# Kernel tuning notes

Measured on AMD Instinct MI355X. Metric: run time of the kernel, lower is better.

Reference implementation:

```python
import jax, jax.numpy as jnp
import numpy as np

ANCHORS = np.array([[10., 13.], [16., 30.], [33., 23.]], dtype=np.float32)
NUM_CLASSES = 80
IMG_W, IMG_H = 416, 416
IGNORE_THR = 0.5
OBJ_SCALE, NOOBJ_SCALE = 1.0, 0.5
EPS = 1e-12


def setup_inputs() -> dict:
    key = jax.random.key(0)
    k1, k2, k3, k4, k5 = jax.random.split(key, 5)
    B, A, C, H, W = 16, 3, NUM_CLASSES, 52, 52
    x = jax.random.normal(k1, (B, A * (C + 5), H, W), dtype=jnp.float32)
    N = 256
    img = jax.random.randint(k2, (N,), 0, B).astype(jnp.float32)
    xy = jax.random.uniform(k3, (N, 2), minval=0.02, maxval=0.98, dtype=jnp.float32)
    wh = jax.random.uniform(k4, (N, 2), minval=0.02, maxval=0.5, dtype=jnp.float32)
    cls = jax.random.randint(k5, (N,), 0, C).astype(jnp.float32)
    target = jnp.concatenate([img[:, None], xy, wh, cls[:, None]], axis=1)
    return {"x": x, "target": target}


def _masked_mse(p, t, m):
    n = jnp.maximum(jnp.sum(m), 1.0)
    return jnp.sum(m * (p - t) ** 2) / n


def _masked_bce(p, t, m):
    p = jnp.clip(p, EPS, 1.0 - EPS)
    n = jnp.maximum(jnp.sum(m), 1.0)
    return jnp.sum(m * (-(t * jnp.log(p) + (1.0 - t) * jnp.log(1.0 - p)))) / n


def _yolo(x, target):
    anchors = jnp.asarray(ANCHORS)
    B, A, C = x.shape[0], anchors.shape[0], NUM_CLASSES
    H, W = x.shape[2], x.shape[3]
    stride_h, stride_w = IMG_H / H, IMG_W / W
    # [B, A, H, W, C+5]
    pred = x.reshape(B, A, C + 5, H, W).transpose(0, 1, 3, 4, 2)
    cx = jax.nn.sigmoid(pred[..., 0])
    cy = jax.nn.sigmoid(pred[..., 1])
    pw = pred[..., 2]
    ph = pred[..., 3]
    pconf = jax.nn.sigmoid(pred[..., 4])
    pcls = jax.nn.sigmoid(pred[..., 5:])

    # ---- detect (boxes use .data in torch -> stop_gradient) ----
    grid_x = jnp.arange(W, dtype=jnp.float32)[None, None, None, :]
    grid_y = jnp.arange(H, dtype=jnp.float32)[None, None, :, None]
    scale_aw = (anchors[:, 0] / stride_w).reshape(1, A, 1, 1)
    scale_ah = (anchors[:, 1] / stride_h).reshape(1, A, 1, 1)
    bx = jax.lax.stop_gradient(cx) + grid_x
    by = jax.lax.stop_gradient(cy) + grid_y
    bw = jnp.exp(jax.lax.stop_gradient(pw)) * scale_aw
    bh = jnp.exp(jax.lax.stop_gradient(ph)) * scale_ah
    boxes = jnp.stack([bx * stride_w, by * stride_h, bw * stride_w, bh * stride_h], -1)
    output = jnp.concatenate(
        [boxes.reshape(B, -1, 4), pconf.reshape(B, -1, 1), pcls.reshape(B, -1, C)], -1)

    # ---- build targets ----
    img_num = target[:, 0].astype(jnp.int32)
    gxc = target[:, 1] * W
    gyc = target[:, 2] * H
    gw = target[:, 3] * W
    gh = target[:, 4] * H
    label = target[:, 5].astype(jnp.int32)
    # wh-IoU of raw pixel anchors vs grid-unit gt (faithful to original, which
    # passes unscaled self.anchors to bbox_wh_iou)
    aw = anchors[:, 0][:, None]  # [A,1]
    ah = anchors[:, 1][:, None]
    inter = jnp.minimum(aw, gw[None, :]) * jnp.minimum(ah, gh[None, :])
    ious = inter / (aw * ah + 1e-16 + gw[None, :] * gh[None, :] - inter)  # [A,N]
    best_index = jnp.argmax(ious, axis=0)  # [N]
    gi = gxc.astype(jnp.int32)
    gj = gyc.astype(jnp.int32)

    shp = (B, A, H, W)
    obj_mask = jnp.zeros(shp, jnp.float32).at[img_num, best_index, gj, gi].set(1.0)
    noobj_mask = jnp.ones(shp, jnp.float32).at[img_num, best_index, gj, gi].set(0.0)
    # zero noobj where any anchor IoU > ignore threshold
    N = target.shape[0]
    anc = jnp.broadcast_to(jnp.arange(A, dtype=jnp.int32)[:, None], (A, N))
    img_b = jnp.broadcast_to(img_num[None, :], (A, N))
    gj_b = jnp.broadcast_to(gj[None, :], (A, N))
    gi_b = jnp.broadcast_to(gi[None, :], (A, N))
    keep = jnp.where(ious > IGNORE_THR, 0.0, 1.0)
    noobj_mask = noobj_mask.at[img_b, anc, gj_b, gi_b].min(keep)

    tx = jnp.zeros(shp, jnp.float32).at[img_num, best_index, gj, gi].set(gxc - jnp.floor(gxc))
    ty = jnp.zeros(shp, jnp.float32).at[img_num, best_index, gj, gi].set(gyc - jnp.floor(gyc))
    tw = jnp.zeros(shp, jnp.float32).at[img_num, best_index, gj, gi].set(
        jnp.log(gw / anchors[best_index, 0] + 1e-16))
    th = jnp.zeros(shp, jnp.float32).at[img_num, best_index, gj, gi].set(
        jnp.log(gh / anchors[best_index, 1] + 1e-16))
    tconf = jnp.zeros(shp, jnp.float32).at[img_num, best_index, gj, gi].set(1.0)
    tcls = jnp.zeros(shp + (C,), jnp.float32).at[img_num, best_index, gj, gi, label].set(1.0)

    # ---- masked losses (replicating original's center_x/self.w bugs) ----
    loss_x = _masked_mse(cx, tx, obj_mask)
    loss_y = _masked_mse(cx, ty, obj_mask)   # original uses center_x for y loss
    loss_w = _masked_mse(pw, tw, obj_mask)
    loss_h = _masked_mse(pw, th, obj_mask)   # original uses self.w for h loss
    loss_conf = (OBJ_SCALE * _masked_bce(pconf, tconf, obj_mask)
                 + NOOBJ_SCALE * _masked_bce(pconf, tconf, noobj_mask))
    cls_mask = jnp.broadcast_to(obj_mask[..., None], tcls.shape)
    loss_cls = _masked_bce(pcls, tcls, cls_mask)
    total = loss_x + loss_y + loss_w + loss_h + loss_conf + loss_cls
    return output, total


def reference(x, target):
    return _yolo(x, target)
```

## Files before the change

kernel.cpp:

```cpp
#include <hip/hip_runtime.h>
#include <math.h>

#define NA 3
#define NC 80
#define CH 85
#define NB 16
#define HH 52
#define WW 52
#define HW 2704
#define HWF4 676
#define NT 256
#define NCELLS (NB*NA*HW)
#define NBMW 4056
#define STRIDE_F 8.0f
#define IGN_THR 0.5f

#define TP 104
#define TF4 26
#define NF4 2210
#define LSTR 105
#define LDSW 8945
#define NBLK 1248
#define NTAIL 269

#define SW(c, l) ((c) * LSTR + (l) + ((c) >> 2))

__device__ __forceinline__ float sigm(float z) { return 1.0f / (1.0f + expf(-z)); }
__device__ __forceinline__ float splus(float z) { return log1pf(expf(z)); }


__global__ __launch_bounds__(256) void fused_kernel(
        const float* __restrict__ x, float* __restrict__ out,
        const float* __restrict__ target, float* __restrict__ acc,
        int* __restrict__ cnts, int* __restrict__ wofs,
        float* __restrict__ wtx, float* __restrict__ wty,
        float* __restrict__ wtw, float* __restrict__ wth,
        int* __restrict__ wlabel, int* __restrict__ zofs,
        float* __restrict__ partials) {
    __shared__ float lds[LDSW];
    __shared__ float red[4];
    int bid = blockIdx.x;
    int t = threadIdx.x;

    if (bid == NBLK) {
        unsigned int* bm = (unsigned int*)lds;
        int* s_keyobj = (int*)lds + NBMW;
        int* s_cnt = (int*)lds + NBMW + NT;
        if (t < 16) acc[t] = 0.0f;
        if (t == 16) cnts[2] = 0;
        if (t == 0) { s_cnt[0] = 0; s_cnt[1] = 0; }
        for (int i = t; i < NBMW; i += 256) bm[i] = 0u;

        const float awc[3] = {10.f, 16.f, 33.f};
        const float ahc[3] = {13.f, 30.f, 23.f};
        float timg = target[t*6 + 0];
        float gxc  = target[t*6 + 1] * (float)WW;
        float gyc  = target[t*6 + 2] * (float)HH;
        float gw   = target[t*6 + 3] * (float)WW;
        float gh   = target[t*6 + 4] * (float)HH;
        int label  = (int)target[t*6 + 5];

        float best_iou = -1.0f;
        int best = 0, ignbits = 0;
        for (int a = 0; a < 3; a++) {
            float inter = fminf(awc[a], gw) * fminf(ahc[a], gh);
            float iou = inter / (awc[a]*ahc[a] + 1e-16f + gw*gh - inter);
            if (iou > best_iou) { best_iou = iou; best = a; }
            if (iou > IGN_THR) ignbits |= (1 << a);
        }
        int img = (int)timg;
        int gi = (int)gxc, gj = (int)gyc;
        int pixel = gj * WW + gi;
        int cellbase = img * (NA * HW) + pixel;
        int keyobj = cellbase + best * HW;
        s_keyobj[t] = keyobj;
        __syncthreads();

        bool dup = false;
        #pragma unroll 8
        for (int m = 0; m < NT; m++) {
            int k = s_keyobj[m];
            dup = dup || (m > t && k == keyobj);
        }
        if (!dup) {
            int p = atomicAdd(&s_cnt[0], 1);
            wofs[p] = (img * NA + best) * (CH * HW) + pixel;
            wtx[p] = gxc - floorf(gxc);
            wty[p] = gyc - floorf(gyc);
            wtw[p] = logf(gw / awc[best] + 1e-16f);
            wth[p] = logf(gh / ahc[best] + 1e-16f);
            wlabel[p] = label;
        }
        for (int a = 0; a < 3; a++) {
            bool flag = (a == best) || ((ignbits >> a) & 1);
            if (flag) {
                int key = cellbase + a * HW;
                unsigned int bit = 1u << (key & 31);
                unsigned int old = atomicOr(&bm[key >> 5], bit);
                if (!(old & bit)) {
                    int p = atomicAdd(&s_cnt[1], 1);
                    zofs[p] = ((img * NA + a) * CH + 4) * HW + pixel;
                }
            }
        }
        __syncthreads();
        if (t == 0) { cnts[0] = s_cnt[0]; cnts[1] = s_cnt[1]; }
        return;
    }

    int chunk = bid % 26;
    int ba    = bid / 26;
    int a     = ba % NA;
    const float awc[3] = {10.f, 16.f, 33.f};
    const float ahc[3] = {13.f, 30.f, 23.f};

    const float4* x4 = (const float4*)x + (size_t)ba * (CH * HWF4)
                                        + chunk * TF4;
    float4 v[9];
    #pragma unroll
    for (int i = 0; i < 9; i++) {
        int idx = t + i * 256;
        if (idx < NF4) {
            int c = idx / TF4, q = idx - c * TF4;
            v[i] = x4[c * HWF4 + q];
        }
    }
    float noobj = 0.0f;
    #pragma unroll
    for (int i = 0; i < 9; i++) {
        int idx = t + i * 256;
        if (idx < NF4) {
            int c = idx / TF4, q = idx - c * TF4;
            float r[4] = {v[i].x, v[i].y, v[i].z, v[i].w};
            #pragma unroll
            for (int k = 0; k < 4; k++) {
                int l = q * 4 + k;
                float z = r[k], o;
                if (c == 0) {
                    int wc = l - ((l >= WW) ? WW : 0);
                    o = (sigm(z) + (float)wc) * STRIDE_F;
                } else if (c == 1) {
                    int hc = chunk * 2 + ((l >= WW) ? 1 : 0);
                    o = (sigm(z) + (float)hc) * STRIDE_F;
                } else if (c == 2) {
                    o = expf(z) * awc[a];
                } else if (c == 3) {
                    o = expf(z) * ahc[a];
                } else {
                    o = sigm(z);
                    if (c == 4) noobj += splus(z);
                }
                lds[SW(c, l)] = o;
            }
        }
    }
    for (int off = 32; off > 0; off >>= 1)
        noobj += __shfl_down(noobj, off, 64);
    if ((t & 63) == 0) red[t >> 6] = noobj;
    __syncthreads();

    float4* o4 = (float4*)out + (size_t)ba * (HW * CH / 4) + chunk * NF4;
    #pragma unroll
    for (int i = 0; i < 9; i++) {
        int j = t + i * 256;
        if (j < NF4) {
            int flat = 4 * j;
            int cell = flat / CH;
            int ch = flat - cell * CH;
            float4 w;
            float* pw = &w.x;
            #pragma unroll
            for (int k = 0; k < 4; k++) {
                int chk = ch + k, cek = cell;
                if (chk >= CH) { chk -= CH; cek += 1; }
                pw[k] = lds[SW(chk, cek)];
            }
            o4[j] = w;
        }
    }
    if (t == 0) partials[bid] = red[0] + red[1] + red[2] + red[3];
}

__global__ __launch_bounds__(64) void tail_kernel(
        const float* __restrict__ x, const int* __restrict__ cnts,
        const int* __restrict__ wofs, const float* __restrict__ wtx,
        const float* __restrict__ wty, const float* __restrict__ wtw,
        const float* __restrict__ wth, const int* __restrict__ wlabel,
        const int* __restrict__ zofs, const float* __restrict__ partials,
        float* __restrict__ acc, int* __restrict__ done,
        float* __restrict__ out_total) {
    int b = blockIdx.x;
    int lane = threadIdx.x;

    if (b < NT) {
        if (b < cnts[0]) {
            int ofs = wofs[b];
            int label = wlabel[b];
            const float* xp = x + ofs;
            float lcls;
            {
                float z = xp[(size_t)(5 + lane) * HW];
                lcls = (lane == label) ? splus(-z) : splus(z);
            }
            if (lane < 16) {
                int c = 64 + lane;
                float z = xp[(size_t)(5 + c) * HW];
                lcls += (c == label) ? splus(-z) : splus(z);
            }
            float other = 0.0f;
            if (lane == 0) {
                float z0 = xp[0];
                float z2 = xp[(size_t)2 * HW];
                float z4 = xp[(size_t)4 * HW];
                float cx = sigm(z0);
                float dx = cx - wtx[b], dy = cx - wty[b];
                float dw = z2 - wtw[b], dh = z2 - wth[b];
                other = dx*dx + dy*dy + dw*dw + dh*dh + splus(-z4);
            }
            for (int off = 32; off > 0; off >>= 1)
                lcls += __shfl_down(lcls, off, 64);
            if (lane == 0) {
                atomicAdd(&acc[1], other);
                atomicAdd(&acc[2], lcls);
            }
        }
    } else if (b < NT + 12) {
        int idx = (b - NT) * 64 + lane;
        float v = 0.0f;
        if (idx < cnts[1]) v = splus(x[zofs[idx]]);
        for (int off = 32; off > 0; off >>= 1)
            v += __shfl_down(v, off, 64);
        if (lane == 0) atomicAdd(&acc[3], v);
    } else {
        float s = 0.0f;
        for (int i = lane; i < NBLK; i += 64) s += partials[i];
        for (int off = 32; off > 0; off >>= 1)
            s += __shfl_down(s, off, 64);
        if (lane == 0) atomicAdd(&acc[0], s);
    }

    __threadfence();
    if (lane == 0) {
        int old = atomicAdd(done, 1);
        if (old == NTAIL - 1) {
            __threadfence();
            float a0 = atomicAdd(&acc[0], 0.0f);
            float a1 = atomicAdd(&acc[1], 0.0f);
            float a2 = atomicAdd(&acc[2], 0.0f);
            float a3 = atomicAdd(&acc[3], 0.0f);
            float wc = (float)cnts[0];
            float n_obj = fmaxf(wc, 1.0f);
            float n_noobj = fmaxf((float)NCELLS - (float)cnts[1], 1.0f);
            float cls_den = fmaxf(80.0f * wc, 1.0f);
            out_total[0] = a1 / n_obj + a2 / cls_den
                         + 0.5f * ((a0 - a3) / n_noobj);
        }
    }
}

extern "C" void kernel_launch(void* const* d_in, const int* in_sizes, int n_in,
                              void* d_out, int out_size, void* d_ws, size_t ws_size,
                              hipStream_t stream) {
    (void)in_sizes; (void)n_in; (void)out_size; (void)ws_size;
    const float* x      = (const float*)d_in[0];
    const float* target = (const float*)d_in[1];
    float* out = (float*)d_out;

    char* ws = (char*)d_ws;
    float* acc      = (float*)(ws + 0);
    int*   cnts     = (int*)  (ws + 64);
    int*   wofs     = (int*)  (ws + 128);
    float* wtx      = (float*)(ws + 1152);
    float* wty      = (float*)(ws + 2176);
    float* wtw      = (float*)(ws + 3200);
    float* wth      = (float*)(ws + 4224);
    int*   wlabel   = (int*)  (ws + 5248);
    int*   zofs     = (int*)  (ws + 6272);
    float* partials = (float*)(ws + 9344);

    fused_kernel<<<NBLK + 1, 256, 0, stream>>>(
        x, out, target, acc, cnts, wofs, wtx, wty, wtw, wth, wlabel, zofs,
        partials);
    tail_kernel<<<NTAIL, 64, 0, stream>>>(
        x, cnts, wofs, wtx, wty, wtw, wth, wlabel, zofs, partials,
        acc, &cnts[2], out + (size_t)NB * NA * HW * CH);
}
```

Measured before the change: 119.4 us.

## Merge tail reduction into main kernel using spin-wait flags instead of second launch

Measured after the change: 185.3 us. +55.2%, slower.

```diff
diff --git a/kernel.cpp b/kernel.cpp
--- a/kernel.cpp
+++ b/kernel.cpp
@@ -20,8 +20,17 @@
 #define NF4 2210
 #define LSTR 105
 #define LDSW 8945
-#define NBLK 1248
-#define NTAIL 269
+#define NDENSE 1248
+
+#define PREP_BID 0
+#define WIN_B0 1
+#define NWINB 64
+#define ZERO_B0 (WIN_B0 + NWINB)
+#define NZEROB 3
+#define DENSE_B0 (ZERO_B0 + NZEROB)
+#define PART_BID (DENSE_B0 + NDENSE)
+#define GRID (PART_BID + 1)
+#define NTAILP (NWINB + NZEROB + 1)
 
 #define SW(c, l) ((c) * LSTR + (l) + ((c) >> 2))
 
@@ -29,25 +38,23 @@
 __device__ __forceinline__ float splus(float z) { return log1pf(expf(z)); }
 
 
-__global__ __launch_bounds__(256) void fused_kernel(
+__global__ __launch_bounds__(256) void yolo_fused(
         const float* __restrict__ x, float* __restrict__ out,
         const float* __restrict__ target, float* __restrict__ acc,
         int* __restrict__ cnts, int* __restrict__ wofs,
         float* __restrict__ wtx, float* __restrict__ wty,
         float* __restrict__ wtw, float* __restrict__ wth,
         int* __restrict__ wlabel, int* __restrict__ zofs,
-        float* __restrict__ partials) {
+        float* __restrict__ partials, float* __restrict__ out_total) {
     __shared__ float lds[LDSW];
     __shared__ float red[4];
     int bid = blockIdx.x;
     int t = threadIdx.x;
 
-    if (bid == NBLK) {
+    if (bid == PREP_BID) {
         unsigned int* bm = (unsigned int*)lds;
         int* s_keyobj = (int*)lds + NBMW;
         int* s_cnt = (int*)lds + NBMW + NT;
-        if (t < 16) acc[t] = 0.0f;
-        if (t == 16) cnts[2] = 0;
         if (t == 0) { s_cnt[0] = 0; s_cnt[1] = 0; }
         for (int i = t; i < NBMW; i += 256) bm[i] = 0u;
 
@@ -103,99 +110,113 @@
                 }
             }
         }
+        __threadfence();
         __syncthreads();
-        if (t == 0) { cnts[0] = s_cnt[0]; cnts[1] = s_cnt[1]; }
+        if (t == 0) {
+            cnts[0] = s_cnt[0]; cnts[1] = s_cnt[1];
+            __threadfence();
+            atomicExch(&cnts[4], 1);
+        }
         return;
     }
 
-    int chunk = bid % 26;
-    int ba    = bid / 26;
-    int a     = ba % NA;
-    const float awc[3] = {10.f, 16.f, 33.f};
-    const float ahc[3] = {13.f, 30.f, 23.f};
-
-    const float4* x4 = (const float4*)x + (size_t)ba * (CH * HWF4)
-                                        + chunk * TF4;
-    float4 v[9];
-    #pragma unroll
-    for (int i = 0; i < 9; i++) {
-        int idx = t + i * 256;
-        if (idx < NF4) {
-            int c = idx / TF4, q = idx - c * TF4;
-            v[i] = x4[c * HWF4 + q];
-        }
-    }
-    float noobj = 0.0f;
-    #pragma unroll
-    for (int i = 0; i < 9; i++) {
-        int idx = t + i * 256;
-        if (idx < NF4) {
-            int c = idx / TF4, q = idx - c * TF4;
-            float r[4] = {v[i].x, v[i].y, v[i].z, v[i].w};
-            #pragma unroll
-            for (int k = 0; k < 4; k++) {
-                int l = q * 4 + k;
-                float z = r[k], o;
-                if (c == 0) {
-                    int wc = l - ((l >= WW) ? WW : 0);
-                    o = (sigm(z) + (float)wc) * STRIDE_F;
-                } else if (c == 1) {
-                    int hc = chunk * 2 + ((l >= WW) ? 1 : 0);
-                    o = (sigm(z) + (float)hc) * STRIDE_F;
-                } else if (c == 2) {
-                    o = expf(z) * awc[a];
-                } else if (c == 3) {
-                    o = expf(z) * ahc[a];
-                } else {
-                    o = sigm(z);
-                    if (c == 4) noobj += splus(z);
+    if (bid >= DENSE_B0 && bid < PART_BID) {
+        int dbid  = bid - DENSE_B0;
+        int chunk = dbid % 26;
+        int ba    = dbid / 26;
+        int a     = ba % NA;
+        const float awc[3] = {10.f, 16.f, 33.f};
+        const float ahc[3] = {13.f, 30.f, 23.f};
+
+        const float4* x4 = (const float4*)x + (size_t)ba * (CH * HWF4)
+                                            + chunk * TF4;
+        float4 v[9];
+        #pragma unroll
+        for (int i = 0; i < 9; i++) {
+            int idx = t + i * 256;
+            if (idx < NF4) {
+                int c = idx / TF4, q = idx - c * TF4;
+                v[i] = x4[c * HWF4 + q];
+            }
+        }
+        float noobj = 0.0f;
+        #pragma unroll
+        for (int i = 0; i < 9; i++) {
+            int idx = t + i * 256;
+            if (idx < NF4) {
+                int c = idx / TF4, q = idx - c * TF4;
+                float r[4] = {v[i].x, v[i].y, v[i].z, v[i].w};
+                #pragma unroll
+                for (int k = 0; k < 4; k++) {
+                    int l = q * 4 + k;
+                    float z = r[k], o;
+                    if (c == 0) {
+                        int wc = l - ((l >= WW) ? WW : 0);
+                        o = (sigm(z) + (float)wc) * STRIDE_F;
+                    } else if (c == 1) {
+                        int hc = chunk * 2 + ((l >= WW) ? 1 : 0);
+                        o = (sigm(z) + (float)hc) * STRIDE_F;
+                    } else if (c == 2) {
+                        o = expf(z) * awc[a];
+                    } else if (c == 3) {
+                        o = expf(z) * ahc[a];
+                    } else {
+                        o = sigm(z);
+                        if (c == 4) noobj += splus(z);
+                    }
+                    lds[SW(c, l)] = o;
                 }
-                lds[SW(c, l)] = o;
-            }
-        }
-    }
-    for (int off = 32; off > 0; off >>= 1)
-        noobj += __shfl_down(noobj, off, 64);
-    if ((t & 63) == 0) red[t >> 6] = noobj;
+            }
+        }
+        for (int off = 32; off > 0; off >>= 1)
+            noobj += __shfl_down(noobj, off, 64);
+        if ((t & 63) == 0) red[t >> 6] = noobj;
+        __syncthreads();
+
+        float4* o4 = (float4*)out + (size_t)ba * (HW * CH / 4) + chunk * NF4;
+        #pragma unroll
+        for (int i = 0; i < 9; i++) {
+            int j = t + i * 256;
+            if (j < NF4) {
+                int flat = 4 * j;
+                int cell = flat / CH;
+                int ch = flat - cell * CH;
+                float4 w;
+                float* pw = &w.x;
+                #pragma unroll
+                for (int k = 0; k < 4; k++) {
+                    int chk = ch + k, cek = cell;
+                    if (chk >= CH) { chk -= CH; cek += 1; }
+                    pw[k] = lds[SW(chk, cek)];
+                }
+                o4[j] = w;
+            }
+        }
+        if (t == 0) {
+            partials[dbid] = red[0] + red[1] + red[2] + red[3];
+            __threadfence();
+            atomicAdd(&cnts[2], 1);
+        }
+        return;
+    }
+
+    if (t == 0) {
+        while (atomicAdd(&cnts[4], 0) == 0)
+            __builtin_amdgcn_s_sleep(8);
+        if (bid == PART_BID) {
+            while (atomicAdd(&cnts[2], 0) < NDENSE)
+                __builtin_amdgcn_s_sleep(16);
+        }
+    }
     __syncthreads();
-
-    float4* o4 = (float4*)out + (size_t)ba * (HW * CH / 4) + chunk * NF4;
-    #pragma unroll
-    for (int i = 0; i < 9; i++) {
-        int j = t + i * 256;
-        if (j < NF4) {
-            int flat = 4 * j;
-            int cell = flat / CH;
-            int ch = flat - cell * CH;
-            float4 w;
-            float* pw = &w.x;
-            #pragma unroll
-            for (int k = 0; k < 4; k++) {
-                int chk = ch + k, cek = cell;
-                if (chk >= CH) { chk -= CH; cek += 1; }
-                pw[k] = lds[SW(chk, cek)];
-            }
-            o4[j] = w;
-        }
-    }
-    if (t == 0) partials[bid] = red[0] + red[1] + red[2] + red[3];
-}
-
-__global__ __launch_bounds__(64) void tail_kernel(
-        const float* __restrict__ x, const int* __restrict__ cnts,
-        const int* __restrict__ wofs, const float* __restrict__ wtx,
-        const float* __restrict__ wty, const float* __restrict__ wtw,
-        const float* __restrict__ wth, const int* __restrict__ wlabel,
-        const int* __restrict__ zofs, const float* __restrict__ partials,
-        float* __restrict__ acc, int* __restrict__ done,
-        float* __restrict__ out_total) {
-    int b = blockIdx.x;
-    int lane = threadIdx.x;
-
-    if (b < NT) {
-        if (b < cnts[0]) {
-            int ofs = wofs[b];
-            int label = wlabel[b];
+    __threadfence();
+
+    if (bid < ZERO_B0) {
+        int wave = t >> 6, lane = t & 63;
+        int w = (bid - WIN_B0) * 4 + wave;
+        if (w < cnts[0]) {
+            int ofs = wofs[w];
+            int label = wlabel[w];
             const float* xp = x + ofs;
             float lcls;
             {
@@ -213,8 +234,8 @@
                 float z2 = xp[(size_t)2 * HW];
                 float z4 = xp[(size_t)4 * HW];
                 float cx = sigm(z0);
-                float dx = cx - wtx[b], dy = cx - wty[b];
-                float dw = z2 - wtw[b], dh = z2 - wth[b];
+                float dx = cx - wtx[w], dy = cx - wty[w];
+                float dw = z2 - wtw[w], dh = z2 - wth[w];
                 other = dx*dx + dy*dy + dw*dw + dh*dh + splus(-z4);
             }
             for (int off = 32; off > 0; off >>= 1)
@@ -224,25 +245,28 @@
                 atomicAdd(&acc[2], lcls);
             }
         }
-    } else if (b < NT + 12) {
-        int idx = (b - NT) * 64 + lane;
+    } else if (bid < DENSE_B0) {
+        int idx = (bid - ZERO_B0) * 256 + t;
         float v = 0.0f;
         if (idx < cnts[1]) v = splus(x[zofs[idx]]);
         for (int off = 32; off > 0; off >>= 1)
             v += __shfl_down(v, off, 64);
-        if (lane == 0) atomicAdd(&acc[3], v);
+        if ((t & 63) == 0) atomicAdd(&acc[3], v);
     } else {
         float s = 0.0f;
-        for (int i = lane; i < NBLK; i += 64) s += partials[i];
+        for (int i = t; i < NDENSE; i += 256) s += partials[i];
         for (int off = 32; off > 0; off >>= 1)
             s += __shfl_down(s, off, 64);
-        if (lane == 0) atomicAdd(&acc[0], s);
-    }
-
+        if ((t & 63) == 0) red[t >> 6] = s;
+        __syncthreads();
+        if (t == 0) atomicAdd(&acc[0], red[0] + red[1] + red[2] + red[3]);
+    }
+
+    __syncthreads();
     __threadfence();
-    if (lane == 0) {
-        int old = atomicAdd(done, 1);
-        if (old == NTAIL - 1) {
+    if (t == 0) {
+        int old = atomicAdd(&cnts[3], 1);
+        if (old == NTAILP - 1) {
             __threadfence();
             float a0 = atomicAdd(&acc[0], 0.0f);
             float a1 = atomicAdd(&acc[1], 0.0f);
@@ -278,10 +302,8 @@
     int*   zofs     = (int*)  (ws + 6272);
     float* partials = (float*)(ws + 9344);
 
-    fused_kernel<<<NBLK + 1, 256, 0, stream>>>(
+    hipMemsetAsync(ws, 0, 96, stream);
+    yolo_fused<<<GRID, 256, 0, stream>>>(
         x, out, target, acc, cnts, wofs, wtx, wty, wtw, wth, wlabel, zofs,
-        partials);
-    tail_kernel<<<NTAIL, 64, 0, stream>>>(
-        x, cnts, wofs, wtx, wty, wtw, wth, wlabel, zofs, partials,
-        acc, &cnts[2], out + (size_t)NB * NA * HW * CH);
+        partials, out + (size_t)NB * NA * HW * CH);
 }
```

## Split target prep into its own kernel and merge sparse losses into main grid

Applied to the files above, without the earlier changes.

Result: slower. 124.2 us (+4.0%).

```diff
diff --git a/kernel.cpp b/kernel.cpp
--- a/kernel.cpp
+++ b/kernel.cpp
@@ -20,8 +20,12 @@
 #define NF4 2210
 #define LSTR 105
 #define LDSW 8945
-#define NBLK 1248
-#define NTAIL 269
+#define NDENSE 1248
+
+#define NWINB 64
+#define NZEROB 3
+#define TAILB (NWINB + NZEROB)
+#define GRID_B (TAILB + NDENSE)
 
 #define SW(c, l) ((c) * LSTR + (l) + ((c) >> 2))
 
@@ -29,173 +33,172 @@
 __device__ __forceinline__ float splus(float z) { return log1pf(expf(z)); }
 
 
-__global__ __launch_bounds__(256) void fused_kernel(
-        const float* __restrict__ x, float* __restrict__ out,
+__global__ __launch_bounds__(256) void prep_kernel(
         const float* __restrict__ target, float* __restrict__ acc,
         int* __restrict__ cnts, int* __restrict__ wofs,
         float* __restrict__ wtx, float* __restrict__ wty,
         float* __restrict__ wtw, float* __restrict__ wth,
-        int* __restrict__ wlabel, int* __restrict__ zofs,
-        float* __restrict__ partials) {
+        int* __restrict__ wlabel, int* __restrict__ zofs) {
+    __shared__ int plds[NBMW + NT + 2];
+    unsigned int* bm = (unsigned int*)plds;
+    int* s_keyobj = plds + NBMW;
+    int* s_cnt = plds + NBMW + NT;
+    int t = threadIdx.x;
+
+    if (t < 16) acc[t] = 0.0f;
+    if (t == 0) { s_cnt[0] = 0; s_cnt[1] = 0; }
+    for (int i = t; i < NBMW; i += 256) bm[i] = 0u;
+
+    const float awc[3] = {10.f, 16.f, 33.f};
+    const float ahc[3] = {13.f, 30.f, 23.f};
+    float timg = target[t*6 + 0];
+    float gxc  = target[t*6 + 1] * (float)WW;
+    float gyc  = target[t*6 + 2] * (float)HH;
+    float gw   = target[t*6 + 3] * (float)WW;
+    float gh   = target[t*6 + 4] * (float)HH;
+    int label  = (int)target[t*6 + 5];
+
+    float best_iou = -1.0f;
+    int best = 0, ignbits = 0;
+    for (int a = 0; a < 3; a++) {
+        float inter = fminf(awc[a], gw) * fminf(ahc[a], gh);
+        float iou = inter / (awc[a]*ahc[a] + 1e-16f + gw*gh - inter);
+        if (iou > best_iou) { best_iou = iou; best = a; }
+        if (iou > IGN_THR) ignbits |= (1 << a);
+    }
+    int img = (int)timg;
+    int gi = (int)gxc, gj = (int)gyc;
+    int pixel = gj * WW + gi;
+    int cellbase = img * (NA * HW) + pixel;
+    int keyobj = cellbase + best * HW;
+    s_keyobj[t] = keyobj;
+    __syncthreads();
+
+    bool dup = false;
+    #pragma unroll 8
+    for (int m = 0; m < NT; m++) {
+        int k = s_keyobj[m];
+        dup = dup || (m > t && k == keyobj);
+    }
+    if (!dup) {
+        int p = atomicAdd(&s_cnt[0], 1);
+        wofs[p] = (img * NA + best) * (CH * HW) + pixel;
+        wtx[p] = gxc - floorf(gxc);
+        wty[p] = gyc - floorf(gyc);
+        wtw[p] = logf(gw / awc[best] + 1e-16f);
+        wth[p] = logf(gh / ahc[best] + 1e-16f);
+        wlabel[p] = label;
+    }
+    for (int a = 0; a < 3; a++) {
+        bool flag = (a == best) || ((ignbits >> a) & 1);
+        if (flag) {
+            int key = cellbase + a * HW;
+            unsigned int bit = 1u << (key & 31);
+            unsigned int old = atomicOr(&bm[key >> 5], bit);
+            if (!(old & bit)) {
+                int p = atomicAdd(&s_cnt[1], 1);
+                zofs[p] = ((img * NA + a) * CH + 4) * HW + pixel;
+            }
+        }
+    }
+    __syncthreads();
+    if (t == 0) { cnts[0] = s_cnt[0]; cnts[1] = s_cnt[1]; }
+}
+
+__global__ __launch_bounds__(256) void main_kernel(
+        const float* __restrict__ x, float* __restrict__ out,
+        float* __restrict__ acc, const int* __restrict__ cnts,
+        const int* __restrict__ wofs, const float* __restrict__ wtx,
+        const float* __restrict__ wty, const float* __restrict__ wtw,
+        const float* __restrict__ wth, const int* __restrict__ wlabel,
+        const int* __restrict__ zofs, float* __restrict__ partials) {
     __shared__ float lds[LDSW];
     __shared__ float red[4];
     int bid = blockIdx.x;
     int t = threadIdx.x;
 
-    if (bid == NBLK) {
-        unsigned int* bm = (unsigned int*)lds;
-        int* s_keyobj = (int*)lds + NBMW;
-        int* s_cnt = (int*)lds + NBMW + NT;
-        if (t < 16) acc[t] = 0.0f;
-        if (t == 16) cnts[2] = 0;
-        if (t == 0) { s_cnt[0] = 0; s_cnt[1] = 0; }
-        for (int i = t; i < NBMW; i += 256) bm[i] = 0u;
-
+    if (bid >= TAILB) {
+        int dbid  = bid - TAILB;
+        int chunk = dbid % 26;
+        int ba    = dbid / 26;
+        int a     = ba % NA;
         const float awc[3] = {10.f, 16.f, 33.f};
         const float ahc[3] = {13.f, 30.f, 23.f};
-        float timg = target[t*6 + 0];
-        float gxc  = target[t*6 + 1] * (float)WW;
-        float gyc  = target[t*6 + 2] * (float)HH;
-        float gw   = target[t*6 + 3] * (float)WW;
-        float gh   = target[t*6 + 4] * (float)HH;
-        int label  = (int)target[t*6 + 5];
-
-        float best_iou = -1.0f;
-        int best = 0, ignbits = 0;
-        for (int a = 0; a < 3; a++) {
-            float inter = fminf(awc[a], gw) * fminf(ahc[a], gh);
-            float iou = inter / (awc[a]*ahc[a] + 1e-16f + gw*gh - inter);
-            if (iou > best_iou) { best_iou = iou; best = a; }
-            if (iou > IGN_THR) ignbits |= (1 << a);
-        }
-        int img = (int)timg;
-        int gi = (int)gxc, gj = (int)gyc;
-        int pixel = gj * WW + gi;
-        int cellbase = img * (NA * HW) + pixel;
-        int keyobj = cellbase + best * HW;
-        s_keyobj[t] = keyobj;
+
+        const float4* x4 = (const float4*)x + (size_t)ba * (CH * HWF4)
+                                            + chunk * TF4;
+        float4 v[9];
+        #pragma unroll
+        for (int i = 0; i < 9; i++) {
+            int idx = t + i * 256;
+            if (idx < NF4) {
+                int c = idx / TF4, q = idx - c * TF4;
+                v[i] = x4[c * HWF4 + q];
+            }
+        }
+        float noobj = 0.0f;
+        #pragma unroll
+        for (int i = 0; i < 9; i++) {
+            int idx = t + i * 256;
+            if (idx < NF4) {
+                int c = idx / TF4, q = idx - c * TF4;
+                float r[4] = {v[i].x, v[i].y, v[i].z, v[i].w};
+                #pragma unroll
+                for (int k = 0; k < 4; k++) {
+                    int l = q * 4 + k;
+                    float z = r[k], o;
+                    if (c == 0) {
+                        int wc = l - ((l >= WW) ? WW : 0);
+                        o = (sigm(z) + (float)wc) * STRIDE_F;
+                    } else if (c == 1) {
+                        int hc = chunk * 2 + ((l >= WW) ? 1 : 0);
+                        o = (sigm(z) + (float)hc) * STRIDE_F;
+                    } else if (c == 2) {
+                        o = expf(z) * awc[a];
+                    } else if (c == 3) {
+                        o = expf(z) * ahc[a];
+                    } else {
+                        o = sigm(z);
+                        if (c == 4) noobj += splus(z);
+                    }
+                    lds[SW(c, l)] = o;
+                }
+            }
+        }
+        for (int off = 32; off > 0; off >>= 1)
+            noobj += __shfl_down(noobj, off, 64);
+        if ((t & 63) == 0) red[t >> 6] = noobj;
         __syncthreads();
 
-        bool dup = false;
-        #pragma unroll 8
-        for (int m = 0; m < NT; m++) {
-            int k = s_keyobj[m];
-            dup = dup || (m > t && k == keyobj);
-        }
-        if (!dup) {
-            int p = atomicAdd(&s_cnt[0], 1);
-            wofs[p] = (img * NA + best) * (CH * HW) + pixel;
-            wtx[p] = gxc - floorf(gxc);
-            wty[p] = gyc - floorf(gyc);
-            wtw[p] = logf(gw / awc[best] + 1e-16f);
-            wth[p] = logf(gh / ahc[best] + 1e-16f);
-            wlabel[p] = label;
-        }
-        for (int a = 0; a < 3; a++) {
-            bool flag = (a == best) || ((ignbits >> a) & 1);
-            if (flag) {
-                int key = cellbase + a * HW;
-                unsigned int bit = 1u << (key & 31);
-                unsigned int old = atomicOr(&bm[key >> 5], bit);
-                if (!(old & bit)) {
-                    int p = atomicAdd(&s_cnt[1], 1);
-                    zofs[p] = ((img * NA + a) * CH + 4) * HW + pixel;
+        float4* o4 = (float4*)out + (size_t)ba * (HW * CH / 4) + chunk * NF4;
+        #pragma unroll
+        for (int i = 0; i < 9; i++) {
+            int j = t + i * 256;
+            if (j < NF4) {
+                int flat = 4 * j;
+                int cell = flat / CH;
+                int ch = flat - cell * CH;
+                float4 w;
+                float* pw = &w.x;
+                #pragma unroll
+                for (int k = 0; k < 4; k++) {
+                    int chk = ch + k, cek = cell;
+                    if (chk >= CH) { chk -= CH; cek += 1; }
+                    pw[k] = lds[SW(chk, cek)];
                 }
-            }
-        }
-        __syncthreads();
-        if (t == 0) { cnts[0] = s_cnt[0]; cnts[1] = s_cnt[1]; }
+                o4[j] = w;
+            }
+        }
+        if (t == 0) partials[dbid] = red[0] + red[1] + red[2] + red[3];
         return;
     }
 
-    int chunk = bid % 26;
-    int ba    = bid / 26;
-    int a     = ba % NA;
-    const float awc[3] = {10.f, 16.f, 33.f};
-    const float ahc[3] = {13.f, 30.f, 23.f};
-
-    const float4* x4 = (const float4*)x + (size_t)ba * (CH * HWF4)
-                                        + chunk * TF4;
-    float4 v[9];
-    #pragma unroll
-    for (int i = 0; i < 9; i++) {
-        int idx = t + i * 256;
-        if (idx < NF4) {
-            int c = idx / TF4, q = idx - c * TF4;
-            v[i] = x4[c * HWF4 + q];
-        }
-    }
-    float noobj = 0.0f;
-    #pragma unroll
-    for (int i = 0; i < 9; i++) {
-        int idx = t + i * 256;
-        if (idx < NF4) {
-            int c = idx / TF4, q = idx - c * TF4;
-            float r[4] = {v[i].x, v[i].y, v[i].z, v[i].w};
-            #pragma unroll
-            for (int k = 0; k < 4; k++) {
-                int l = q * 4 + k;
-                float z = r[k], o;
-                if (c == 0) {
-                    int wc = l - ((l >= WW) ? WW : 0);
-                    o = (sigm(z) + (float)wc) * STRIDE_F;
-                } else if (c == 1) {
-                    int hc = chunk * 2 + ((l >= WW) ? 1 : 0);
-                    o = (sigm(z) + (float)hc) * STRIDE_F;
-                } else if (c == 2) {
-                    o = expf(z) * awc[a];
-                } else if (c == 3) {
-                    o = expf(z) * ahc[a];
-                } else {
-                    o = sigm(z);
-                    if (c == 4) noobj += splus(z);
-                }
-                lds[SW(c, l)] = o;
-            }
-        }
-    }
-    for (int off = 32; off > 0; off >>= 1)
-        noobj += __shfl_down(noobj, off, 64);
-    if ((t & 63) == 0) red[t >> 6] = noobj;
-    __syncthreads();
-
-    float4* o4 = (float4*)out + (size_t)ba * (HW * CH / 4) + chunk * NF4;
-    #pragma unroll
-    for (int i = 0; i < 9; i++) {
-        int j = t + i * 256;
-        if (j < NF4) {
-            int flat = 4 * j;
-            int cell = flat / CH;
-            int ch = flat - cell * CH;
-            float4 w;
-            float* pw = &w.x;
-            #pragma unroll
-            for (int k = 0; k < 4; k++) {
-                int chk = ch + k, cek = cell;
-                if (chk >= CH) { chk -= CH; cek += 1; }
-                pw[k] = lds[SW(chk, cek)];
-            }
-            o4[j] = w;
-        }
-    }
-    if (t == 0) partials[bid] = red[0] + red[1] + red[2] + red[3];
-}
-
-__global__ __launch_bounds__(64) void tail_kernel(
-        const float* __restrict__ x, const int* __restrict__ cnts,
-        const int* __restrict__ wofs, const float* __restrict__ wtx,
-        const float* __restrict__ wty, const float* __restrict__ wtw,
-        const float* __restrict__ wth, const int* __restrict__ wlabel,
-        const int* __restrict__ zofs, const float* __restrict__ partials,
-        float* __restrict__ acc, int* __restrict__ done,
-        float* __restrict__ out_total) {
-    int b = blockIdx.x;
-    int lane = threadIdx.x;
-
-    if (b < NT) {
-        if (b < cnts[0]) {
-            int ofs = wofs[b];
-            int label = wlabel[b];
+    if (bid < NWINB) {
+        int wave = t >> 6, lane = t & 63;
+        int w = bid * 4 + wave;
+        if (w < cnts[0]) {
+            int ofs = wofs[w];
+            int label = wlabel[w];
             const float* xp = x + ofs;
             float lcls;
             {
@@ -213,8 +216,8 @@
                 float z2 = xp[(size_t)2 * HW];
                 float z4 = xp[(size_t)4 * HW];
                 float cx = sigm(z0);
-                float dx = cx - wtx[b], dy = cx - wty[b];
-                float dw = z2 - wtw[b], dh = z2 - wth[b];
+                float dx = cx - wtx[w], dy = cx - wty[w];
+                float dw = z2 - wtw[w], dh = z2 - wth[w];
                 other = dx*dx + dy*dy + dw*dw + dh*dh + splus(-z4);
             }
             for (int off = 32; off > 0; off >>= 1)
@@ -224,37 +227,37 @@
                 atomicAdd(&acc[2], lcls);
             }
         }
-    } else if (b < NT + 12) {
-        int idx = (b - NT) * 64 + lane;
-        float v = 0.0f;
-        if (idx < cnts[1]) v = splus(x[zofs[idx]]);
+    } else {
+        int idx = (bid - NWINB) * 256 + t;
+        float vv = 0.0f;
+        if (idx < cnts[1]) vv = splus(x[zofs[idx]]);
         for (int off = 32; off > 0; off >>= 1)
-            v += __shfl_down(v, off, 64);
-        if (lane == 0) atomicAdd(&acc[3], v);
-    } else {
-        float s = 0.0f;
-        for (int i = lane; i < NBLK; i += 64) s += partials[i];
-        for (int off = 32; off > 0; off >>= 1)
-            s += __shfl_down(s, off, 64);
-        if (lane == 0) atomicAdd(&acc[0], s);
-    }
-
-    __threadfence();
-    if (lane == 0) {
-        int old = atomicAdd(done, 1);
-        if (old == NTAIL - 1) {
-            __threadfence();
-            float a0 = atomicAdd(&acc[0], 0.0f);
-            float a1 = atomicAdd(&acc[1], 0.0f);
-            float a2 = atomicAdd(&acc[2], 0.0f);
-            float a3 = atomicAdd(&acc[3], 0.0f);
-            float wc = (float)cnts[0];
-            float n_obj = fmaxf(wc, 1.0f);
-            float n_noobj = fmaxf((float)NCELLS - (float)cnts[1], 1.0f);
-            float cls_den = fmaxf(80.0f * wc, 1.0f);
-            out_total[0] = a1 / n_obj + a2 / cls_den
-                         + 0.5f * ((a0 - a3) / n_noobj);
-        }
+            vv += __shfl_down(vv, off, 64);
+        if ((t & 63) == 0) atomicAdd(&acc[3], vv);
+    }
+}
+
+__global__ __launch_bounds__(256) void finalize_kernel(
+        const float* __restrict__ partials, const float* __restrict__ acc,
+        const int* __restrict__ cnts, float* __restrict__ out_total) {
+    __shared__ float red[4];
+    int t = threadIdx.x;
+    float s = 0.0f;
+    for (int i = t; i < NDENSE; i += 256) s += partials[i];
+    for (int off = 32; off > 0; off >>= 1)
+        s += __shfl_down(s, off, 64);
+    if ((t & 63) == 0) red[t >> 6] = s;
+    __syncthreads();
+    if (t == 0) {
+        float a0 = red[0] + red[1] + red[2] + red[3];
+        float a1 = acc[1], a2 = acc[2], a3 = acc[3];
+        float wc = (float)cnts[0];
+        float zc = (float)cnts[1];
+        float n_obj = fmaxf(wc, 1.0f);
+        float n_noobj = fmaxf((float)NCELLS - zc, 1.0f);
+        float cls_den = fmaxf(80.0f * wc, 1.0f);
+        out_total[0] = a1 / n_obj + a2 / cls_den
+                     + 0.5f * ((a0 - a3) / n_noobj);
     }
 }
 
@@ -278,10 +281,10 @@
     int*   zofs     = (int*)  (ws + 6272);
     float* partials = (float*)(ws + 9344);
 
-    fused_kernel<<<NBLK + 1, 256, 0, stream>>>(
-        x, out, target, acc, cnts, wofs, wtx, wty, wtw, wth, wlabel, zofs,
-        partials);
-    tail_kernel<<<NTAIL, 64, 0, stream>>>(
-        x, cnts, wofs, wtx, wty, wtw, wth, wlabel, zofs, partials,
-        acc, &cnts[2], out + (size_t)NB * NA * HW * CH);
-}
+    prep_kernel<<<1, 256, 0, stream>>>(
+        target, acc, cnts, wofs, wtx, wty, wtw, wth, wlabel, zofs);
+    main_kernel<<<GRID_B, 256, 0, stream>>>(
+        x, out, acc, cnts, wofs, wtx, wty, wtw, wth, wlabel, zofs, partials);
+    finalize_kernel<<<1, 256, 0, stream>>>(
+        partials, acc, cnts, out + (size_t)NB * NA * HW * CH);
+}
```
